# Performance work log

Hardware: AMD Instinct MI355X
Metric: run time of the kernel (lower is better)

## Reference

```python
import jax, jax.numpy as jnp
import numpy as np
from jax import lax

D_MODEL = 256
DEPTH = 2
DI = 512        # d_inner = expand * d_model
N = 16          # d_state
DCONV = 4
DTR = 16        # dt_rank = ceil(d_model/16)
BSZ = 32
T = 2048
EPS = 1e-5


def setup_inputs() -> dict:
    key = jax.random.key(0)
    ks = jax.random.split(key, 13)
    s = 0.02
    x = jax.random.normal(ks[0], (BSZ, T, D_MODEL), jnp.float32)
    mask = jax.random.randint(ks[1], (BSZ, T), 0, 2) > 0
    ln_w = 1.0 + 0.1 * jax.random.normal(ks[2], (DEPTH, D_MODEL), jnp.float32)
    ln_b = 0.1 * jax.random.normal(ks[3], (DEPTH, D_MODEL), jnp.float32)
    in_proj_w = s * jax.random.normal(ks[4], (DEPTH, 2 * DI, D_MODEL), jnp.float32)
    conv_w = s * jax.random.normal(ks[5], (DEPTH, DI, DCONV), jnp.float32)
    conv_b = s * jax.random.normal(ks[6], (DEPTH, DI), jnp.float32)
    x_proj_w = s * jax.random.normal(ks[7], (DEPTH, DTR + 2 * N, DI), jnp.float32)
    dt_proj_w = s * jax.random.normal(ks[8], (DEPTH, DI, DTR), jnp.float32)
    dt_proj_b = s * jax.random.normal(ks[9], (DEPTH, DI), jnp.float32)
    # A = -exp(A_log) in (-e^3, -1): stable decaying dynamics
    A_log = jax.random.uniform(ks[10], (DEPTH, DI, N), jnp.float32, 0.0, 3.0)
    skip_D = s * jax.random.normal(ks[11], (DEPTH, DI), jnp.float32)
    out_proj_w = s * jax.random.normal(ks[12], (DEPTH, D_MODEL, DI), jnp.float32)
    return {"x": x, "mask": mask, "ln_w": ln_w, "ln_b": ln_b,
            "in_proj_w": in_proj_w, "conv_w": conv_w, "conv_b": conv_b,
            "x_proj_w": x_proj_w, "dt_proj_w": dt_proj_w, "dt_proj_b": dt_proj_b,
            "A_log": A_log, "skip_D": skip_D, "out_proj_w": out_proj_w}


def _layernorm(x, w, b):
    mu = jnp.mean(x, axis=-1, keepdims=True)
    var = jnp.mean(jnp.square(x - mu), axis=-1, keepdims=True)
    return (x - mu) * lax.rsqrt(var + EPS) * w + b


def _mamba(x, in_proj_w, conv_w, conv_b, x_proj_w, dt_proj_w, dt_proj_b, A_log, skip_D, out_proj_w):
    Bsz, L, _ = x.shape
    xz = jnp.einsum('btd,ed->bte', x, in_proj_w)      # (B,T,2*DI)
    u, z = jnp.split(xz, 2, axis=-1)                  # (B,T,DI) each
    # causal depthwise conv1d, kernel size DCONV
    up = jnp.pad(u, ((0, 0), (DCONV - 1, 0), (0, 0)))
    uc = conv_b
    for k in range(DCONV):
        uc = uc + up[:, k:k + L, :] * conv_w[:, k]
    u = jax.nn.silu(uc)
    x_dbl = jnp.einsum('btd,ed->bte', u, x_proj_w)    # (B,T,DTR+2N)
    dt_in, Bm, Cm = jnp.split(x_dbl, [DTR, DTR + N], axis=-1)
    dt = jax.nn.softplus(jnp.einsum('btr,dr->btd', dt_in, dt_proj_w) + dt_proj_b)  # (B,T,DI)
    A = -jnp.exp(A_log)                               # (DI,N)

    def step(h, inp):
        dt_t, B_t, C_t, u_t = inp                     # (B,DI),(B,N),(B,N),(B,DI)
        dA = jnp.exp(dt_t[..., None] * A)             # (B,DI,N)
        h = dA * h + (dt_t * u_t)[..., None] * B_t[:, None, :]
        y = jnp.einsum('bdn,bn->bd', h, C_t)
        return h, y

    h0 = jnp.zeros((Bsz, DI, N), x.dtype)
    xs = (dt.transpose(1, 0, 2), Bm.transpose(1, 0, 2),
          Cm.transpose(1, 0, 2), u.transpose(1, 0, 2))
    _, ys = lax.scan(step, h0, xs)                    # (T,B,DI)
    y = ys.transpose(1, 0, 2) + u * skip_D
    y = y * jax.nn.silu(z)
    return jnp.einsum('btd,ed->bte', y, out_proj_w)   # (B,T,d_model)


def reference(x, mask, ln_w, ln_b, in_proj_w, conv_w, conv_b, x_proj_w,
              dt_proj_w, dt_proj_b, A_log, skip_D, out_proj_w):
    m = mask[..., None].astype(x.dtype)
    x = x * m
    for i in range(DEPTH):
        h = _mamba(_layernorm(x, ln_w[i], ln_b[i]), in_proj_w[i], conv_w[i],
                   conv_b[i], x_proj_w[i], dt_proj_w[i], dt_proj_b[i],
                   A_log[i], skip_D[i], out_proj_w[i])
        x = (x + h) * m   # dropout in eval mode = identity
    return x
```

## Files before the change

### kernel.cpp

```cpp
#include <hip/hip_runtime.h>
#include <cstdint>

#define LOG2E 1.4426950408889634f
#define BCH 16
#define RC  (BCH * 2048)

typedef __attribute__((ext_vector_type(8))) short short8;
typedef __attribute__((ext_vector_type(4))) float f32x4;
typedef __attribute__((ext_vector_type(4))) unsigned short ush4;
typedef __attribute__((ext_vector_type(8))) unsigned short ush8;

__device__ __forceinline__ float b2f(unsigned short u) {
  union { unsigned int u; float f; } c; c.u = ((unsigned int)u) << 16; return c.f;
}
__device__ __forceinline__ unsigned short f2b(float f) {
  union { float f; unsigned int u; } c; c.f = f;
  unsigned int r = c.u + 0x7FFFu + ((c.u >> 16) & 1u);
  return (unsigned short)(r >> 16);
}
__device__ __forceinline__ float ex2(float x) { return __builtin_amdgcn_exp2f(x); }
__device__ __forceinline__ f32x4 exp2v(f32x4 v) {
  f32x4 r; r.x = ex2(v.x); r.y = ex2(v.y); r.z = ex2(v.z); r.w = ex2(v.w);
  return r;
}

__device__ __forceinline__ f32x4 ld4(const float* p) {
  f32x4 r;
  asm volatile("global_load_dwordx4 %0, %1, off" : "=v"(r) : "v"(p));
  return r;
}

__device__ __forceinline__ void gl2lds16(void* l, const void* g) {
  __builtin_amdgcn_global_load_lds(
      (const __attribute__((address_space(1))) void*)g,
      (__attribute__((address_space(3))) void*)l, 16, 0, 0);
}

__global__ __launch_bounds__(256) void prep_weights(
    const float* __restrict__ inw, const float* __restrict__ xw,
    const float* __restrict__ ow, const float* __restrict__ alog,
    unsigned short* __restrict__ inwb, unsigned short* __restrict__ xwb,
    unsigned short* __restrict__ owb, float* __restrict__ AA) {
  int gid = blockIdx.x * 256 + threadIdx.x;
  const int n_in = 2 * 1024 * 256;
  const int n_x  = 2 * 48 * 512;
  const int n_o  = 2 * 256 * 512;
  const int n_a  = 2 * 512 * 16;
  if (gid < n_in) { inwb[gid] = f2b(inw[gid]); return; }
  gid -= n_in;
  if (gid < n_x) { xwb[gid] = f2b(xw[gid]); return; }
  gid -= n_x;
  if (gid < n_o) { owb[gid] = f2b(ow[gid]); return; }
  gid -= n_o;
  if (gid < n_a) { AA[gid] = -__expf(alog[gid]) * LOG2E; }
}

__global__ __launch_bounds__(256) void mask_x(
    const float* __restrict__ x, const int* __restrict__ mask,
    float* __restrict__ X) {
  int gid = blockIdx.x * 256 + threadIdx.x;
  int row = gid >> 8;
  X[gid] = mask[row] ? x[gid] : 0.f;
}

__global__ __launch_bounds__(256) void ln_fwd(
    const float* __restrict__ X, const float* __restrict__ w,
    const float* __restrict__ b, unsigned short* __restrict__ XN) {
  int wv = threadIdx.x >> 6, ln = threadIdx.x & 63;
  long row = (long)blockIdx.x * 4 + wv;
  f32x4 v = ((const f32x4*)(X + row * 256))[ln];
  float s = v.x + v.y + v.z + v.w;
  float s2 = v.x * v.x + v.y * v.y + v.z * v.z + v.w * v.w;
  #pragma unroll
  for (int o = 32; o > 0; o >>= 1) {
    s += __shfl_xor(s, o, 64);
    s2 += __shfl_xor(s2, o, 64);
  }
  float mu = s * (1.f / 256.f);
  float var = s2 * (1.f / 256.f) - mu * mu;
  float rst = rsqrtf(var + 1e-5f);
  f32x4 wv4 = ((const f32x4*)w)[ln];
  f32x4 bv4 = ((const f32x4*)b)[ln];
  ush4 o4;
  o4.x = f2b((v.x - mu) * rst * wv4.x + bv4.x);
  o4.y = f2b((v.y - mu) * rst * wv4.y + bv4.y);
  o4.z = f2b((v.z - mu) * rst * wv4.z + bv4.z);
  o4.w = f2b((v.w - mu) * rst * wv4.w + bv4.w);
  ((ush4*)(XN + row * 256))[ln] = o4;
}

__global__ __launch_bounds__(256) void gemm128(
    const unsigned short* __restrict__ A, const unsigned short* __restrict__ B,
    unsigned short* __restrict__ OutU, unsigned short* __restrict__ OutZ,
    int N, int K) {
  __shared__ unsigned short As[128 * 32];
  __shared__ unsigned short Bs[128 * 32];
  const int tid = threadIdx.x;
  const int wave = tid >> 6, lane = tid & 63;
  const int m0 = blockIdx.x * 128, n0 = blockIdx.y * 128;
  const int wm = (wave >> 1) * 64, wn = (wave & 1) * 64;

  f32x4 acc[4][4];
  #pragma unroll
  for (int i = 0; i < 4; i++)
    #pragma unroll
    for (int j = 0; j < 4; j++)
      #pragma unroll
      for (int r = 0; r < 4; r++) acc[i][j][r] = 0.f;

  const int srow = wave * 32 + (lane >> 2);
  const int skcol = (lane & 3) * 8;
  unsigned short* AsW = &As[srow * 32 + skcol];
  unsigned short* BsW = &Bs[srow * 32 + skcol];
  const unsigned short* Ag = A + (long)(m0 + srow) * K + skcol;
  const unsigned short* Bg = B + (long)(n0 + srow) * K + skcol;

  const int fr = lane & 15, fk = (lane >> 4) * 8;

  for (int k0 = 0; k0 < K; k0 += 32) {
    gl2lds16(AsW,            Ag + k0);
    gl2lds16(AsW + 16 * 32,  Ag + (long)16 * K + k0);
    gl2lds16(BsW,            Bg + k0);
    gl2lds16(BsW + 16 * 32,  Bg + (long)16 * K + k0);
    __syncthreads();
    short8 af[4], bf[4];
    #pragma unroll
    for (int i = 0; i < 4; i++) {
      af[i] = *(const short8*)&As[(wm + i * 16 + fr) * 32 + fk];
      bf[i] = *(const short8*)&Bs[(wn + i * 16 + fr) * 32 + fk];
    }
    #pragma unroll
    for (int i = 0; i < 4; i++)
      #pragma unroll
      for (int j = 0; j < 4; j++)
        acc[i][j] = __builtin_amdgcn_mfma_f32_16x16x32_bf16(af[i], bf[j], acc[i][j], 0, 0, 0);
    __syncthreads();
  }

  const int cl = lane & 15, rq = (lane >> 4) * 4;
  #pragma unroll
  for (int i = 0; i < 4; i++)
    #pragma unroll
    for (int j = 0; j < 4; j++) {
      int col = n0 + wn + j * 16 + cl;
      #pragma unroll
      for (int r = 0; r < 4; r++) {
        int row = m0 + wm + i * 16 + rq + r;
        float v = acc[i][j][r];
        if (col < 512) OutU[(long)row * 512 + col] = f2b(v);
        else           OutZ[(long)row * 512 + (col - 512)] = f2b(v);
      }
    }
}

__global__ __launch_bounds__(256) void gemm64(
    const unsigned short* __restrict__ A, const unsigned short* __restrict__ B,
    const float* __restrict__ Xres, float* __restrict__ OutF,
    const int* __restrict__ mask, int N, int K) {
  __shared__ unsigned short As[64 * 32];
  __shared__ unsigned short Bs[128 * 32];
  const int tid = threadIdx.x;
  const int wave = tid >> 6, lane = tid & 63;
  const int m0 = blockIdx.x * 64, n0 = blockIdx.y * 128;
  const int wm = (wave >> 1) * 32, wn = (wave & 1) * 64;

  f32x4 acc[2][4];
  #pragma unroll
  for (int i = 0; i < 2; i++)
    #pragma unroll
    for (int j = 0; j < 4; j++)
      #pragma unroll
      for (int r = 0; r < 4; r++) acc[i][j][r] = 0.f;

  const int srow = wave * 32 + (lane >> 2);
  const int skcol = (lane & 3) * 8;
  unsigned short* AsW = &As[srow * 32 + skcol];
  unsigned short* BsW = &Bs[srow * 32 + skcol];
  const unsigned short* Ag = A + (long)(m0 + srow) * K + skcol;
  const unsigned short* Bg = B + (long)(n0 + srow) * K + skcol;

  const int fr = lane & 15, fk = (lane >> 4) * 8;

  for (int k0 = 0; k0 < K; k0 += 32) {
    if (wave < 2) {
      gl2lds16(AsW,            Ag + k0);
      gl2lds16(AsW + 16 * 32,  Ag + (long)16 * K + k0);
    }
    gl2lds16(BsW,            Bg + k0);
    gl2lds16(BsW + 16 * 32,  Bg + (long)16 * K + k0);
    __syncthreads();
    short8 af[2], bf[4];
    #pragma unroll
    for (int i = 0; i < 2; i++)
      af[i] = *(const short8*)&As[(wm + i * 16 + fr) * 32 + fk];
    #pragma unroll
    for (int j = 0; j < 4; j++)
      bf[j] = *(const short8*)&Bs[(wn + j * 16 + fr) * 32 + fk];
    #pragma unroll
    for (int i = 0; i < 2; i++)
      #pragma unroll
      for (int j = 0; j < 4; j++)
        acc[i][j] = __builtin_amdgcn_mfma_f32_16x16x32_bf16(af[i], bf[j], acc[i][j], 0, 0, 0);
    __syncthreads();
  }

  const int cl = lane & 15, rq = (lane >> 4) * 4;
  #pragma unroll
  for (int i = 0; i < 2; i++)
    #pragma unroll
    for (int j = 0; j < 4; j++) {
      int col = n0 + wn + j * 16 + cl;
      #pragma unroll
      for (int r = 0; r < 4; r++) {
        int row = m0 + wm + i * 16 + rq + r;
        long idx = (long)row * N + col;
        OutF[idx] = Xres[idx] + (mask[row] ? acc[i][j][r] : 0.f);
      }
    }
}

__global__ __launch_bounds__(256) void gemm_n48(
    const unsigned short* __restrict__ A, const unsigned short* __restrict__ B,
    float* __restrict__ Out, int K) {
  __shared__ unsigned short As[128 * 32];
  __shared__ unsigned short Bs[48 * 32];
  const int tid = threadIdx.x;
  const int wave = tid >> 6, lane = tid & 63;
  const int m0 = blockIdx.x * 128;
  const int wm = wave * 32;

  f32x4 acc[2][3];
  #pragma unroll
  for (int i = 0; i < 2; i++)
    #pragma unroll
    for (int j = 0; j < 3; j++)
      #pragma unroll
      for (int r = 0; r < 4; r++) acc[i][j][r] = 0.f;

  const int srow = wave * 32 + (lane >> 2);
  const int skcol = (lane & 3) * 8;
  unsigned short* AsW = &As[srow * 32 + skcol];
  const unsigned short* Ag = A + (long)(m0 + srow) * K + skcol;
  const int brow = wave * 16 + (lane >> 2);
  unsigned short* BsW = &Bs[brow * 32 + skcol];
  const unsigned short* Bg = B + (long)brow * K + skcol;

  const int fr = lane & 15, fk = (lane >> 4) * 8;

  for (int k0 = 0; k0 < K; k0 += 32) {
    gl2lds16(AsW,           Ag + k0);
    gl2lds16(AsW + 16 * 32, Ag + (long)16 * K + k0);
    if (wave < 3) gl2lds16(BsW, Bg + k0);
    __syncthreads();
    short8 af[2], bf[3];
    #pragma unroll
    for (int i = 0; i < 2; i++)
      af[i] = *(const short8*)&As[(wm + i * 16 + fr) * 32 + fk];
    #pragma unroll
    for (int j = 0; j < 3; j++)
      bf[j] = *(const short8*)&Bs[(j * 16 + fr) * 32 + fk];
    #pragma unroll
    for (int i = 0; i < 2; i++)
      #pragma unroll
      for (int j = 0; j < 3; j++)
        acc[i][j] = __builtin_amdgcn_mfma_f32_16x16x32_bf16(af[i], bf[j], acc[i][j], 0, 0, 0);
    __syncthreads();
  }

  const int cl = lane & 15, rq = (lane >> 4) * 4;
  #pragma unroll
  for (int i = 0; i < 2; i++)
    #pragma unroll
    for (int j = 0; j < 3; j++) {
      int col = j * 16 + cl;
      #pragma unroll
      for (int r = 0; r < 4; r++) {
        int row = m0 + wm + i * 16 + rq + r;
        Out[(long)row * 48 + col] = acc[i][j][r];
      }
    }
}

__global__ __launch_bounds__(256, 4) void conv_silu(
    const unsigned short* __restrict__ Upre, const float* __restrict__ cw,
    const float* __restrict__ cb, unsigned short* __restrict__ U) {
  int gid = blockIdx.x * 256 + threadIdx.x;
  int d8 = gid & 63;
  int row = gid >> 6;
  int t = row & 2047;
  int d0 = d8 * 8;
  f32x4 cwv[8];
  #pragma unroll
  for (int di = 0; di < 8; di++) cwv[di] = ((const f32x4*)(cw + (d0 + di) * 4))[0];
  f32x4 cbv0 = ((const f32x4*)(cb + d0))[0];
  f32x4 cbv1 = ((const f32x4*)(cb + d0))[1];
  float acc[8] = {cbv0.x, cbv0.y, cbv0.z, cbv0.w, cbv1.x, cbv1.y, cbv1.z, cbv1.w};
  #pragma unroll
  for (int k = 0; k < 4; k++) {
    int tt = t + k - 3;
    if (tt >= 0) {
      ush8 uv = *(const ush8*)(Upre + (long)(row + k - 3) * 512 + d0);
      #pragma unroll
      for (int di = 0; di < 8; di++)
        acc[di] = fmaf(b2f(uv[di]), cwv[di][k], acc[di]);
    }
  }
  ush8 o;
  #pragma unroll
  for (int di = 0; di < 8; di++) {
    float sg = 1.f / (1.f + __expf(-acc[di]));
    o[di] = f2b(acc[di] * sg);
  }
  *(ush8*)(U + (long)row * 512 + d0) = o;
}

__global__ __launch_bounds__(256, 4) void scan_p1(
    const unsigned short* __restrict__ U, const float* __restrict__ XD,
    const float* __restrict__ AA, const float* __restrict__ dtw,
    const float* __restrict__ dtb, float* __restrict__ HCH,
    float* __restrict__ DTS) {
  int gid = blockIdx.x * 256 + threadIdx.x;
  int d = gid & 511;
  int bc = gid >> 9;
  int c = bc & 63, b = bc >> 6;
  f32x4 aa0 = ld4(AA + d * 16),      aa1 = ld4(AA + d * 16 + 4),
        aa2 = ld4(AA + d * 16 + 8),  aa3 = ld4(AA + d * 16 + 12);
  f32x4 w0 = ld4(dtw + d * 16),      w1 = ld4(dtw + d * 16 + 4),
        w2 = ld4(dtw + d * 16 + 8),  w3 = ld4(dtw + d * 16 + 12);
  asm volatile("s_waitcnt vmcnt(0)"
               : "+v"(aa0), "+v"(aa1), "+v"(aa2), "+v"(aa3),
                 "+v"(w0), "+v"(w1), "+v"(w2), "+v"(w3));
  f32x4 h0 = {0.f,0.f,0.f,0.f}, h1 = h0, h2 = h0, h3 = h0;
  float bias = dtb[d];
  float dts = 0.f;
  int row = b * 2048 + c * 32;
  const unsigned short* Up = U + (long)row * 512 + d;
  for (int tt = 0; tt < 32; tt++, row++, Up += 512) {
    int off = __builtin_amdgcn_readfirstlane(row * 48);
    const f32x4* xs = (const f32x4*)(XD + off);
    f32x4 x0 = xs[0], x1 = xs[1], x2 = xs[2], x3 = xs[3];
    f32x4 B0 = xs[4], B1 = xs[5], B2 = xs[6], B3 = xs[7];
    f32x4 pp = x0 * w0 + x1 * w1 + x2 * w2 + x3 * w3;
    float s = bias + pp.x + pp.y + pp.z + pp.w;
    float e = __expf(-fabsf(s));
    float dt = fmaxf(s, 0.f) + __logf(1.f + e);
    float du = dt * b2f(*Up);
    h0 = exp2v(dt * aa0) * h0 + du * B0;
    h1 = exp2v(dt * aa1) * h1 + du * B1;
    h2 = exp2v(dt * aa2) * h2 + du * B2;
    h3 = exp2v(dt * aa3) * h3 + du * B3;
    dts += dt;
  }
  f32x4* hp = (f32x4*)(HCH + (long)gid * 16);
  hp[0] = h0; hp[1] = h1; hp[2] = h2; hp[3] = h3;
  DTS[gid] = dts;
}

__global__ __launch_bounds__(256) void scan_p2(
    float* __restrict__ HCH, const float* __restrict__ DTS,
    const float* __restrict__ AA) {
  int gid = blockIdx.x * 256 + threadIdx.x;
  int n = gid & 15;
  int d = (gid >> 4) & 511;
  int b = gid >> 13;
  float aa = AA[d * 16 + n];
  float hrun = 0.f;
  for (int c = 0; c < 64; c++) {
    long base = ((long)b * 64 + c) * 512 + d;
    long idx = base * 16 + n;
    float hend = HCH[idx];
    float P = ex2(DTS[base] * aa);
    HCH[idx] = hrun;
    hrun = fmaf(P, hrun, hend);
  }
}

__global__ __launch_bounds__(256, 4) void scan_p3(
    const unsigned short* __restrict__ U, const unsigned short* __restrict__ Z,
    const float* __restrict__ XD, const float* __restrict__ AA,
    const float* __restrict__ dtw, const float* __restrict__ dtb,
    const float* __restrict__ HCH, const float* __restrict__ skD,
    unsigned short* __restrict__ Y) {
  int gid = blockIdx.x * 256 + threadIdx.x;
  int d = gid & 511;
  int bc = gid >> 9;
  int c = bc & 63, b = bc >> 6;
  f32x4 aa0 = ld4(AA + d * 16),      aa1 = ld4(AA + d * 16 + 4),
        aa2 = ld4(AA + d * 16 + 8),  aa3 = ld4(AA + d * 16 + 12);
  f32x4 w0 = ld4(dtw + d * 16),      w1 = ld4(dtw + d * 16 + 4),
        w2 = ld4(dtw + d * 16 + 8),  w3 = ld4(dtw + d * 16 + 12);
  asm volatile("s_waitcnt vmcnt(0)"
               : "+v"(aa0), "+v"(aa1), "+v"(aa2), "+v"(aa3),
                 "+v"(w0), "+v"(w1), "+v"(w2), "+v"(w3));
  const f32x4* hp = (const f32x4*)(HCH + (long)gid * 16);
  f32x4 h0 = hp[0], h1 = hp[1], h2 = hp[2], h3 = hp[3];
  float bias = dtb[d];
  float sD = skD[d];
  int row = b * 2048 + c * 32;
  const unsigned short* Up = U + (long)row * 512 + d;
  const unsigned short* Zp = Z + (long)row * 512 + d;
  unsigned short* Yp = Y + (long)row * 512 + d;
  for (int tt = 0; tt < 32; tt++, row++, Up += 512, Zp += 512, Yp += 512) {
    int off = __builtin_amdgcn_readfirstlane(row * 48);
    const f32x4* xs = (const f32x4*)(XD + off);
    f32x4 x0 = xs[0], x1 = xs[1], x2 = xs[2], x3 = xs[3];
    f32x4 B0 = xs[4], B1 = xs[5], B2 = xs[6], B3 = xs[7];
    f32x4 C0 = xs[8], C1 = xs[9], C2 = xs[10], C3 = xs[11];
    f32x4 pp = x0 * w0 + x1 * w1 + x2 * w2 + x3 * w3;
    float s = bias + pp.x + pp.y + pp.z + pp.w;
    float e = __expf(-fabsf(s));
    float dt = fmaxf(s, 0.f) + __logf(1.f + e);
    float u = b2f(*Up);
    float du = dt * u;
    h0 = exp2v(dt * aa0) * h0 + du * B0;
    h1 = exp2v(dt * aa1) * h1 + du * B1;
    h2 = exp2v(dt * aa2) * h2 + du * B2;
    h3 = exp2v(dt * aa3) * h3 + du * B3;
    f32x4 yv = h0 * C0 + h1 * C1 + h2 * C2 + h3 * C3;
    float y = yv.x + yv.y + yv.z + yv.w + u * sD;
    float z = b2f(*Zp);
    float sg = z / (1.f + __expf(-z));
    *Yp = f2b(y * sg);
  }
}

extern "C" void kernel_launch(void* const* d_in, const int* in_sizes, int n_in,
                              void* d_out, int out_size, void* d_ws, size_t ws_size,
                              hipStream_t stream) {
  const float* x        = (const float*)d_in[0];
  const int*   mask     = (const int*)d_in[1];
  const float* ln_w     = (const float*)d_in[2];
  const float* ln_b     = (const float*)d_in[3];
  const float* in_proj  = (const float*)d_in[4];
  const float* conv_w   = (const float*)d_in[5];
  const float* conv_b   = (const float*)d_in[6];
  const float* x_proj   = (const float*)d_in[7];
  const float* dt_w     = (const float*)d_in[8];
  const float* dt_b     = (const float*)d_in[9];
  const float* A_log    = (const float*)d_in[10];
  const float* skip_D   = (const float*)d_in[11];
  const float* out_proj = (const float*)d_in[12];
  float* X = (float*)d_out;

  char* p = (char*)d_ws;
  auto alloc = [&](size_t n) { char* r = p; p += (n + 255) & ~(size_t)255; return r; };
  unsigned short* WBin  = (unsigned short*)alloc((size_t)2 * 1024 * 256 * 2);
  unsigned short* WBx   = (unsigned short*)alloc((size_t)2 * 48 * 512 * 2);
  unsigned short* WBout = (unsigned short*)alloc((size_t)2 * 256 * 512 * 2);
  float*          AA    = (float*)alloc((size_t)2 * 512 * 16 * 4);
  char* R_XN   = alloc((size_t)RC * 256 * 2);
  char* R_UPRE = alloc((size_t)RC * 512 * 2);
  char* R_Z    = alloc((size_t)RC * 512 * 2);
  char* R_U    = alloc((size_t)RC * 512 * 2);

  unsigned short* XN   = (unsigned short*)R_XN;
  float*          XD   = (float*)R_XN;
  float*          DTS  = (float*)(R_XN + 8388608);
  unsigned short* Upre = (unsigned short*)R_UPRE;
  float*          HCH  = (float*)R_UPRE;
  unsigned short* Z    = (unsigned short*)R_Z;
  unsigned short* U    = (unsigned short*)R_U;

  prep_weights<<<3328, 256, 0, stream>>>(in_proj, x_proj, out_proj, A_log,
                                         WBin, WBx, WBout, AA);
  mask_x<<<65536, 256, 0, stream>>>(x, mask, X);

  for (int ch = 0; ch < 2; ch++) {
    const long row0 = (long)ch * RC;
    float* Xc = X + row0 * 256;
    const int* maskc = mask + row0;
    for (int i = 0; i < 2; i++) {
      ln_fwd<<<RC / 4, 256, 0, stream>>>(Xc, ln_w + i * 256, ln_b + i * 256, XN);
      gemm128<<<dim3(RC / 128, 8), 256, 0, stream>>>(XN, WBin + i * 262144,
          Upre, Z, 1024, 256);
      conv_silu<<<RC / 4, 256, 0, stream>>>(Upre, conv_w + i * 2048,
          conv_b + i * 512, U);
      gemm_n48<<<RC / 128, 256, 0, stream>>>(U, WBx + i * 24576, XD, 512);
      scan_p1<<<BCH * 128, 256, 0, stream>>>(U, XD, AA + i * 8192,
          dt_w + i * 8192, dt_b + i * 512, HCH, DTS);
      scan_p2<<<BCH * 32, 256, 0, stream>>>(HCH, DTS, AA + i * 8192);
      scan_p3<<<BCH * 128, 256, 0, stream>>>(U, Z, XD, AA + i * 8192,
          dt_w + i * 8192, dt_b + i * 512, HCH, skip_D + i * 512, U);
      gemm64<<<dim3(RC / 64, 2), 256, 0, stream>>>(U, WBout + i * 131072,
          Xc, Xc, maskc, 256, 512);
    }
  }
}
```

Measured before the change: 1.203 ms.

## Cache dt in fp16 between scan passes and swizzle GEMM blocks across XCDs

scan_p1 now writes the softplus dt for every (row, channel) to an fp16 workspace buffer, and scan_p3 reads it back instead of recomputing the dt_proj dot product, exp and log. The cached path is used only when the workspace is large enough. Separately, gemm128 and gemm64 remap their block indices so that consecutive blocks on each XCD work on nearby M tiles, aiming for better L2 reuse. The trade-off is an extra 32 MB of memory traffic per layer chunk, plus fp16 rounding of dt that could change accuracy slightly.

```diff
diff --git a/kernel.cpp b/kernel.cpp
--- a/kernel.cpp
+++ b/kernel.cpp
@@ -97,7 +97,10 @@
   __shared__ unsigned short Bs[128 * 32];
   const int tid = threadIdx.x;
   const int wave = tid >> 6, lane = tid & 63;
-  const int m0 = blockIdx.x * 128, n0 = blockIdx.y * 128;
+  const int lin = blockIdx.x + blockIdx.y * 256;
+  const int xcd = lin & 7, idx = lin >> 3;
+  const int m0 = (xcd * 32 + (idx >> 3)) * 128;
+  const int n0 = (idx & 7) * 128;
   const int wm = (wave >> 1) * 64, wn = (wave & 1) * 64;
 
   f32x4 acc[4][4];
@@ -161,7 +164,10 @@
   __shared__ unsigned short Bs[128 * 32];
   const int tid = threadIdx.x;
   const int wave = tid >> 6, lane = tid & 63;
-  const int m0 = blockIdx.x * 64, n0 = blockIdx.y * 128;
+  const int lin = blockIdx.x + blockIdx.y * 512;
+  const int xcd = lin & 7, idx = lin >> 3;
+  const int m0 = (xcd * 64 + (idx >> 1)) * 64;
+  const int n0 = (idx & 1) * 128;
   const int wm = (wave >> 1) * 32, wn = (wave & 1) * 64;
 
   f32x4 acc[2][4];
@@ -213,8 +219,8 @@
       #pragma unroll
       for (int r = 0; r < 4; r++) {
         int row = m0 + wm + i * 16 + rq + r;
-        long idx = (long)row * N + col;
-        OutF[idx] = Xres[idx] + (mask[row] ? acc[i][j][r] : 0.f);
+        long idx2 = (long)row * N + col;
+        OutF[idx2] = Xres[idx2] + (mask[row] ? acc[i][j][r] : 0.f);
       }
     }
 }
@@ -314,11 +320,12 @@
   *(ush8*)(U + (long)row * 512 + d0) = o;
 }
 
+template<int DTM>
 __global__ __launch_bounds__(256, 4) void scan_p1(
     const unsigned short* __restrict__ U, const float* __restrict__ XD,
     const float* __restrict__ AA, const float* __restrict__ dtw,
     const float* __restrict__ dtb, float* __restrict__ HCH,
-    float* __restrict__ DTS) {
+    float* __restrict__ DTS, _Float16* __restrict__ DTH) {
   int gid = blockIdx.x * 256 + threadIdx.x;
   int d = gid & 511;
   int bc = gid >> 9;
@@ -335,7 +342,8 @@
   float dts = 0.f;
   int row = b * 2048 + c * 32;
   const unsigned short* Up = U + (long)row * 512 + d;
-  for (int tt = 0; tt < 32; tt++, row++, Up += 512) {
+  _Float16* DTp = DTH + (long)row * 512 + d;
+  for (int tt = 0; tt < 32; tt++, row++, Up += 512, DTp += 512) {
     int off = __builtin_amdgcn_readfirstlane(row * 48);
     const f32x4* xs = (const f32x4*)(XD + off);
     f32x4 x0 = xs[0], x1 = xs[1], x2 = xs[2], x3 = xs[3];
@@ -344,6 +352,7 @@
     float s = bias + pp.x + pp.y + pp.z + pp.w;
     float e = __expf(-fabsf(s));
     float dt = fmaxf(s, 0.f) + __logf(1.f + e);
+    if (DTM) *DTp = (_Float16)dt;
     float du = dt * b2f(*Up);
     h0 = exp2v(dt * aa0) * h0 + du * B0;
     h1 = exp2v(dt * aa1) * h1 + du * B1;
@@ -375,41 +384,54 @@
   }
 }
 
+template<int DTM>
 __global__ __launch_bounds__(256, 4) void scan_p3(
     const unsigned short* __restrict__ U, const unsigned short* __restrict__ Z,
     const float* __restrict__ XD, const float* __restrict__ AA,
     const float* __restrict__ dtw, const float* __restrict__ dtb,
     const float* __restrict__ HCH, const float* __restrict__ skD,
-    unsigned short* __restrict__ Y) {
+    unsigned short* __restrict__ Y, const _Float16* __restrict__ DTH) {
   int gid = blockIdx.x * 256 + threadIdx.x;
   int d = gid & 511;
   int bc = gid >> 9;
   int c = bc & 63, b = bc >> 6;
   f32x4 aa0 = ld4(AA + d * 16),      aa1 = ld4(AA + d * 16 + 4),
         aa2 = ld4(AA + d * 16 + 8),  aa3 = ld4(AA + d * 16 + 12);
-  f32x4 w0 = ld4(dtw + d * 16),      w1 = ld4(dtw + d * 16 + 4),
-        w2 = ld4(dtw + d * 16 + 8),  w3 = ld4(dtw + d * 16 + 12);
-  asm volatile("s_waitcnt vmcnt(0)"
-               : "+v"(aa0), "+v"(aa1), "+v"(aa2), "+v"(aa3),
-                 "+v"(w0), "+v"(w1), "+v"(w2), "+v"(w3));
+  f32x4 w0, w1, w2, w3;
+  if (!DTM) {
+    w0 = ld4(dtw + d * 16);     w1 = ld4(dtw + d * 16 + 4);
+    w2 = ld4(dtw + d * 16 + 8); w3 = ld4(dtw + d * 16 + 12);
+    asm volatile("s_waitcnt vmcnt(0)"
+                 : "+v"(aa0), "+v"(aa1), "+v"(aa2), "+v"(aa3),
+                   "+v"(w0), "+v"(w1), "+v"(w2), "+v"(w3));
+  } else {
+    asm volatile("s_waitcnt vmcnt(0)"
+                 : "+v"(aa0), "+v"(aa1), "+v"(aa2), "+v"(aa3));
+  }
   const f32x4* hp = (const f32x4*)(HCH + (long)gid * 16);
   f32x4 h0 = hp[0], h1 = hp[1], h2 = hp[2], h3 = hp[3];
-  float bias = dtb[d];
+  float bias = DTM ? 0.f : dtb[d];
   float sD = skD[d];
   int row = b * 2048 + c * 32;
   const unsigned short* Up = U + (long)row * 512 + d;
   const unsigned short* Zp = Z + (long)row * 512 + d;
   unsigned short* Yp = Y + (long)row * 512 + d;
-  for (int tt = 0; tt < 32; tt++, row++, Up += 512, Zp += 512, Yp += 512) {
+  const _Float16* DTp = DTH + (long)row * 512 + d;
+  for (int tt = 0; tt < 32; tt++, row++, Up += 512, Zp += 512, Yp += 512, DTp += 512) {
     int off = __builtin_amdgcn_readfirstlane(row * 48);
     const f32x4* xs = (const f32x4*)(XD + off);
-    f32x4 x0 = xs[0], x1 = xs[1], x2 = xs[2], x3 = xs[3];
     f32x4 B0 = xs[4], B1 = xs[5], B2 = xs[6], B3 = xs[7];
     f32x4 C0 = xs[8], C1 = xs[9], C2 = xs[10], C3 = xs[11];
-    f32x4 pp = x0 * w0 + x1 * w1 + x2 * w2 + x3 * w3;
-    float s = bias + pp.x + pp.y + pp.z + pp.w;
-    float e = __expf(-fabsf(s));
-    float dt = fmaxf(s, 0.f) + __logf(1.f + e);
+    float dt;
+    if (DTM) {
+      dt = (float)*DTp;
+    } else {
+      f32x4 x0 = xs[0], x1 = xs[1], x2 = xs[2], x3 = xs[3];
+      f32x4 pp = x0 * w0 + x1 * w1 + x2 * w2 + x3 * w3;
+      float s = bias + pp.x + pp.y + pp.z + pp.w;
+      float e = __expf(-fabsf(s));
+      dt = fmaxf(s, 0.f) + __logf(1.f + e);
+    }
     float u = b2f(*Up);
     float du = dt * u;
     h0 = exp2v(dt * aa0) * h0 + du * B0;
@@ -452,6 +474,7 @@
   char* R_UPRE = alloc((size_t)RC * 512 * 2);
   char* R_Z    = alloc((size_t)RC * 512 * 2);
   char* R_U    = alloc((size_t)RC * 512 * 2);
+  char* R_DT   = alloc((size_t)RC * 512 * 2);
 
   unsigned short* XN   = (unsigned short*)R_XN;
   float*          XD   = (float*)R_XN;
@@ -460,6 +483,9 @@
   float*          HCH  = (float*)R_UPRE;
   unsigned short* Z    = (unsigned short*)R_Z;
   unsigned short* U    = (unsigned short*)R_U;
+  _Float16*       DTH  = (_Float16*)R_DT;
+
+  const bool use_dt = ws_size >= (size_t)((char*)p - (char*)d_ws);
 
   prep_weights<<<3328, 256, 0, stream>>>(in_proj, x_proj, out_proj, A_log,
                                          WBin, WBx, WBout, AA);
@@ -476,11 +502,21 @@
       conv_silu<<<RC / 4, 256, 0, stream>>>(Upre, conv_w + i * 2048,
           conv_b + i * 512, U);
       gemm_n48<<<RC / 128, 256, 0, stream>>>(U, WBx + i * 24576, XD, 512);
-      scan_p1<<<BCH * 128, 256, 0, stream>>>(U, XD, AA + i * 8192,
-          dt_w + i * 8192, dt_b + i * 512, HCH, DTS);
+      if (use_dt) {
+        scan_p1<1><<<BCH * 128, 256, 0, stream>>>(U, XD, AA + i * 8192,
+            dt_w + i * 8192, dt_b + i * 512, HCH, DTS, DTH);
+      } else {
+        scan_p1<0><<<BCH * 128, 256, 0, stream>>>(U, XD, AA + i * 8192,
+            dt_w + i * 8192, dt_b + i * 512, HCH, DTS, DTH);
+      }
       scan_p2<<<BCH * 32, 256, 0, stream>>>(HCH, DTS, AA + i * 8192);
-      scan_p3<<<BCH * 128, 256, 0, stream>>>(U, Z, XD, AA + i * 8192,
-          dt_w + i * 8192, dt_b + i * 512, HCH, skip_D + i * 512, U);
+      if (use_dt) {
+        scan_p3<1><<<BCH * 128, 256, 0, stream>>>(U, Z, XD, AA + i * 8192,
+            dt_w + i * 8192, dt_b + i * 512, HCH, skip_D + i * 512, U, DTH);
+      } else {
+        scan_p3<0><<<BCH * 128, 256, 0, stream>>>(U, Z, XD, AA + i * 8192,
+            dt_w + i * 8192, dt_b + i * 512, HCH, skip_D + i * 512, U, DTH);
+      }
       gemm64<<<dim3(RC / 64, 2), 256, 0, stream>>>(U, WBout + i * 131072,
           Xc, Xc, maskc, 256, 512);
     }
```

After: 1.122 ms. 6.8% less time.
